# Optimization experiments

Hardware: AMD Instinct MI355X
Metric: run time of the kernel (lower is better)

The kernel has to match this reference:

```python
import jax, jax.numpy as jnp
import numpy as np

B, O, D = 4096, 256, 256  # batch, size_out (rules), size_in (features)


def setup_inputs() -> dict:
    key = jax.random.key(0)
    k1, k2, k3, k4, k5 = jax.random.split(key, 5)
    return {
        "x": jax.random.normal(k1, (B, D), dtype=jnp.float32),
        "scales": jax.random.normal(k2, (O, D), dtype=jnp.float32),
        # strict upper triangle holds the packed rot vectors (original inits them to zeros;
        # small values keep the quadratic form well conditioned)
        "rots": jax.random.normal(k3, (O, D, D), dtype=jnp.float32) * 0.02,
        "centroids": jax.random.normal(k4, (O, D, 1), dtype=jnp.float32),
        "b": jax.random.uniform(k5, (O,), dtype=jnp.float32, minval=0.5, maxval=1.5),
    }


def reference(x, scales, rots, centroids, b):
    # Build symmetric transform A[o] = diag(scales[o]) + triu(rots[o],1) + triu(rots[o],1)^T
    # (equivalent to the loop of diag_embed(r_i, i+1) + mirrored lower diagonal).
    upper = jnp.triu(rots, 1)                                   # [O,D,D]
    A = upper + jnp.swapaxes(upper, -1, -2)
    A = A + jnp.eye(D, dtype=scales.dtype) * scales[:, None, :]  # diag_embed(scales)
    # Augmented affine map: mul[o,i,b'] = A[o] @ x[b'] + centroid[o,i]; const row dropped
    # since only the first size_in rows feed the norm.
    y = jnp.einsum('bj,oij->boi', x, A) + centroids[..., 0][None, :, :]  # [B,O,D]
    rx = jnp.sqrt(jnp.sum(y * y, axis=-1))                      # L2 norm over D -> [B,O]
    return 1.0 / (1.0 + rx ** (2.0 * b))                        # bell membership [B,O]
```

## Files before the change

### kernel.cpp

```cpp
#include <hip/hip_runtime.h>
#include <cstdint>
#include <cmath>

#define Bn 4096
#define Dn 256
#define On 256

typedef __bf16 v8bf __attribute__((ext_vector_type(8)));
typedef float  v16f __attribute__((ext_vector_type(16)));
typedef unsigned short us8 __attribute__((ext_vector_type(8)));

__device__ __forceinline__ unsigned short f2bf(float f) {
    unsigned int u = __builtin_bit_cast(unsigned int, f);
    unsigned int r = (u + 0x7fffu + ((u >> 16) & 1u)) >> 16;
    return (unsigned short)r;
}

__device__ __forceinline__ void gl_lds16(const void* g, void* l) {
    __builtin_amdgcn_global_load_lds(
        (const __attribute__((address_space(1))) void*)(uintptr_t)g,
        (__attribute__((address_space(3))) void*)(uintptr_t)l, 16, 0, 0);
}

__global__ __launch_bounds__(256) void prep_x(const float* __restrict__ x,
                                              unsigned short* __restrict__ xbT) {
    __shared__ float t[64][68];
    const int tid = threadIdx.x;
    const int bb = blockIdx.x >> 2;
    const int kb = blockIdx.x & 3;
    const int b0 = bb * 64;
#pragma unroll
    for (int s = 0; s < 4; ++s) {
        const int idx = s * 256 + tid;
        const int r = idx >> 4, c4 = idx & 15;
        const float4 v = *(const float4*)(x + (size_t)(b0 + r) * Dn + kb * 64 + c4 * 4);
        *(float4*)&t[r][c4 * 4] = v;
    }
    __syncthreads();
    const int lane = tid & 63, wv = tid >> 6;
#pragma unroll
    for (int s = 0; s < 2; ++s) {
        const int kcl = s * 4 + wv;
        us8 u;
#pragma unroll
        for (int q = 0; q < 8; ++q) u[q] = f2bf(t[lane][kcl * 8 + q]);
        *(us8*)(xbT + ((size_t)(kb * 8 + kcl) * Bn + b0 + lane) * 8) = u;
    }
}

template <int TI, int TJ>
__device__ __forceinline__ void extract_pair(const float* T, v8bf (&af)[2][16],
                                             const float (&sc2)[2],
                                             int wv, int lane) {
    const int l31 = lane & 31, hw = lane >> 5;
    if (TI == TJ) {
        if (wv == TI) {
#pragma unroll
            for (int mt = 0; mt < 2; ++mt) {
                const int r = mt * 32 + l31;
                const int mr = (r & 7) << 2;
#pragma unroll
                for (int kq = 0; kq < 4; ++kq) {
                    us8 u;
#pragma unroll
                    for (int q = 0; q < 8; ++q) {
                        const int c = kq * 16 + hw * 8 + q;
                        const float v = (r < c) ? T[r * 64 + (c ^ mr)]
                                      : ((r > c) ? T[c * 64 + (r ^ ((c & 7) << 2))]
                                                 : sc2[mt]);
                        u[q] = f2bf(v);
                    }
                    af[mt][TJ * 4 + kq] = __builtin_bit_cast(v8bf, u);
                }
            }
        }
    } else {
        if (wv == TI) {
#pragma unroll
            for (int mt = 0; mt < 2; ++mt) {
                const int r = mt * 32 + l31;
                const int mr = (r & 7) << 2;
#pragma unroll
                for (int kq = 0; kq < 4; ++kq) {
                    const int c0 = kq * 16 + hw * 8;
                    const float4 a = *(const float4*)&T[r * 64 + (c0 ^ mr)];
                    const float4 b = *(const float4*)&T[r * 64 + ((c0 + 4) ^ mr)];
                    us8 u;
                    u[0] = f2bf(a.x); u[1] = f2bf(a.y); u[2] = f2bf(a.z); u[3] = f2bf(a.w);
                    u[4] = f2bf(b.x); u[5] = f2bf(b.y); u[6] = f2bf(b.z); u[7] = f2bf(b.w);
                    af[mt][TJ * 4 + kq] = __builtin_bit_cast(v8bf, u);
                }
            }
        } else if (wv == TJ) {
#pragma unroll
            for (int mt = 0; mt < 2; ++mt) {
                const int cL = mt * 32 + l31;
#pragma unroll
                for (int kq = 0; kq < 4; ++kq) {
                    us8 u;
#pragma unroll
                    for (int q = 0; q < 8; ++q) {
                        const int rL = kq * 16 + hw * 8 + q;
                        u[q] = f2bf(T[rL * 64 + (cL ^ ((rL & 7) << 2))]);
                    }
                    af[mt][TI * 4 + kq] = __builtin_bit_cast(v8bf, u);
                }
            }
        }
    }
}

#define WAITV(N)                                              \
    do {                                                      \
        asm volatile("s_waitcnt vmcnt(" #N ")" ::: "memory"); \
        __builtin_amdgcn_sched_barrier(0);                    \
    } while (0)
#define LGKM0()                                               \
    do {                                                      \
        asm volatile("s_waitcnt lgkmcnt(0)" ::: "memory");    \
        __builtin_amdgcn_sched_barrier(0);                    \
    } while (0)
#define BARF()                                                \
    do {                                                      \
        __builtin_amdgcn_sched_barrier(0);                    \
        __builtin_amdgcn_s_barrier();                         \
        __builtin_amdgcn_sched_barrier(0);                    \
    } while (0)

#define STAGE_T(TIv, TJv, DST)                                               \
    do {                                                                     \
        const float* s_ = rbase + (TIv) * (64 * Dn) + (TJv) * 64;            \
        _Pragma("unroll")                                                    \
        for (int s = 0; s < 4; ++s) {                                        \
            const int idx = s * 256 + tid;                                   \
            const int r = idx >> 4, c4 = idx & 15;                           \
            gl_lds16(s_ + (size_t)r * Dn + ((c4 ^ (r & 7)) * 4),             \
                     (DST) + idx * 4);                                       \
        }                                                                    \
    } while (0)

#define XSTAGE(BUF, B0)                                                      \
    do {                                                                     \
        _Pragma("unroll")                                                    \
        for (int s = 0; s < 8; ++s) {                                        \
            gl_lds16(xbT + ((size_t)(s * 4 + wv) * Bn + (B0) + lane) * 8,    \
                     &Xs[BUF][s * 256 + tid][0]);                            \
        }                                                                    \
    } while (0)

__global__ __launch_bounds__(256, 2) void fuzzy_main(
    const float* __restrict__ rots, const float* __restrict__ scales,
    const unsigned short* __restrict__ xbT, const float* __restrict__ cent,
    const float* __restrict__ bvals, float* __restrict__ out) {
    __shared__ __align__(16) unsigned short Xs[2][2048][8];
    __shared__ float ssbuf[2][4][64];
    __shared__ float centL[Dn];

    const int tid  = threadIdx.x;
    const int lane = tid & 63;
    const int wv   = tid >> 6;
    const int l31  = lane & 31, hw = lane >> 5;
    const int Lb = blockIdx.x;
    const int o     = (Lb & 7) * 32 + ((Lb >> 3) & 31);
    const int bhalf = Lb >> 8;

    centL[tid] = cent[o * Dn + tid];
    float sc2[2];
#pragma unroll
    for (int mt = 0; mt < 2; ++mt)
        sc2[mt] = scales[o * Dn + wv * 64 + mt * 32 + l31];
    const float bv = bvals[o];

    WAITV(0);

    float* const S0 = (float*)&Xs[1][0][0];
    float* const S1 = S0 + 4096;
    float* const S2 = (float*)&Xs[0][0][0];
    float* const S3 = S2 + 4096;
    const float* const rbase = rots + ((size_t)o << 16);

    v8bf af[2][16];

    STAGE_T(0, 1, S0); STAGE_T(2, 3, S1);
    STAGE_T(0, 2, S2); STAGE_T(1, 3, S3);
    WAITV(8); BARF();
    extract_pair<0, 1>(S0, af, sc2, wv, lane);
    extract_pair<2, 3>(S1, af, sc2, wv, lane);
    LGKM0(); BARF();
    STAGE_T(0, 3, S0); STAGE_T(1, 2, S1);
    WAITV(8); BARF();
    extract_pair<0, 2>(S2, af, sc2, wv, lane);
    extract_pair<1, 3>(S3, af, sc2, wv, lane);
    LGKM0(); BARF();
    STAGE_T(0, 0, S2); STAGE_T(1, 1, S3);
    WAITV(8); BARF();
    extract_pair<0, 3>(S0, af, sc2, wv, lane);
    extract_pair<1, 2>(S1, af, sc2, wv, lane);
    LGKM0(); BARF();
    STAGE_T(2, 2, S0); STAGE_T(3, 3, S1);
    WAITV(8); BARF();
    extract_pair<0, 0>(S2, af, sc2, wv, lane);
    extract_pair<1, 1>(S3, af, sc2, wv, lane);
    LGKM0(); BARF();
    WAITV(0); BARF();
    extract_pair<2, 2>(S0, af, sc2, wv, lane);
    extract_pair<3, 3>(S1, af, sc2, wv, lane);
    LGKM0(); BARF();

    XSTAGE(0, bhalf * 2048);
    __syncthreads();

    for (int it = 0; it < 32; ++it) {
        const int buf = it & 1;
        const int b0  = bhalf * 2048 + it * 64;
        if (it < 31) XSTAGE(buf ^ 1, b0 + 64);

        if (it > 0 && lane < 16) {
            const int bl = wv * 16 + lane;
            const float ssq = ssbuf[buf ^ 1][0][bl] + ssbuf[buf ^ 1][1][bl] +
                              ssbuf[buf ^ 1][2][bl] + ssbuf[buf ^ 1][3][bl];
            out[(size_t)(b0 - 64 + bl) * On + o] =
                1.0f / (1.0f + exp2f(bv * log2f(ssq)));
        }

        v16f acc[2][2];
#pragma unroll
        for (int mt = 0; mt < 2; ++mt)
#pragma unroll
            for (int nt = 0; nt < 2; ++nt)
#pragma unroll
                for (int rg = 0; rg < 16; ++rg) acc[mt][nt][rg] = 0.f;

#pragma unroll
        for (int ks = 0; ks < 16; ++ks) {
            v8bf xf[2];
#pragma unroll
            for (int nt = 0; nt < 2; ++nt)
                xf[nt] = *(const v8bf*)&Xs[buf][(ks * 2 + hw) * 64 + nt * 32 + l31][0];
#pragma unroll
            for (int mt = 0; mt < 2; ++mt)
#pragma unroll
                for (int nt = 0; nt < 2; ++nt)
                    acc[mt][nt] = __builtin_amdgcn_mfma_f32_32x32x16_bf16(
                        af[mt][ks], xf[nt], acc[mt][nt], 0, 0, 0);
        }

#pragma unroll
        for (int nt = 0; nt < 2; ++nt) {
            float v = 0.f;
#pragma unroll
            for (int mt = 0; mt < 2; ++mt)
#pragma unroll
                for (int rg = 0; rg < 16; ++rg) {
                    const float y = acc[mt][nt][rg] +
                        centL[wv * 64 + mt * 32 + (rg & 3) + 8 * (rg >> 2) + 4 * hw];
                    v += y * y;
                }
            v += __shfl_xor(v, 32);
            if (lane < 32) ssbuf[buf][wv][nt * 32 + lane] = v;
        }
        __syncthreads();
    }
    if (lane < 16) {
        const int bl = wv * 16 + lane;
        const float ssq = ssbuf[1][0][bl] + ssbuf[1][1][bl] +
                          ssbuf[1][2][bl] + ssbuf[1][3][bl];
        out[(size_t)(bhalf * 2048 + 31 * 64 + bl) * On + o] =
            1.0f / (1.0f + exp2f(bv * log2f(ssq)));
    }
}

__global__ void fallback_kernel(const float* __restrict__ x, const float* __restrict__ scales,
                                const float* __restrict__ rots, const float* __restrict__ cent,
                                const float* __restrict__ bvals, float* __restrict__ out) {
    const int b = blockIdx.x * blockDim.x + threadIdx.x;
    const int o = blockIdx.y;
    if (b >= Bn) return;
    const float* R  = rots + (size_t)o * Dn * Dn;
    const float* xv = x + (size_t)b * Dn;
    float ss = 0.f;
    for (int i = 0; i < Dn; ++i) {
        float a = cent[o * Dn + i];
        for (int j = 0; j < Dn; ++j) {
            const float w = (j > i) ? R[i * Dn + j]
                          : ((j < i) ? R[j * Dn + i] : scales[o * Dn + i]);
            a += w * xv[j];
        }
        ss += a * a;
    }
    out[(size_t)b * On + o] = 1.f / (1.f + powf(ss, bvals[o]));
}

extern "C" void kernel_launch(void* const* d_in, const int* in_sizes, int n_in,
                              void* d_out, int out_size, void* d_ws, size_t ws_size,
                              hipStream_t stream) {
    const float* x         = (const float*)d_in[0];
    const float* scales    = (const float*)d_in[1];
    const float* rots      = (const float*)d_in[2];
    const float* centroids = (const float*)d_in[3];
    const float* bvals     = (const float*)d_in[4];
    float* out = (float*)d_out;

    const size_t needX = (size_t)Bn * Dn * sizeof(unsigned short);

    if (ws_size >= needX) {
        unsigned short* xbT = (unsigned short*)d_ws;
        prep_x<<<dim3(256), 256, 0, stream>>>(x, xbT);
        fuzzy_main<<<dim3(512), 256, 0, stream>>>(rots, scales, xbT, centroids, bvals, out);
    } else {
        fallback_kernel<<<dim3(Bn / 256, On), 256, 0, stream>>>(x, scales, rots, centroids,
                                                                bvals, out);
    }
}
```

Before: 225.9 us.

## Software-pipeline MFMA tiles with epilogue norm reduction across iterations

The main loop now splits each 64-column batch tile into two 32-column halves. The squared-norm epilogue of one half's accumulators is interleaved with the MFMA chain of the other half, so VALU work overlaps matrix-core work instead of running after it. The partial-sum buffer becomes triple-buffered to carry results across iterations. The X staging pointers are precomputed and incremented to cut address arithmetic. This adds a skewed prologue and epilogue and keeps an extra accumulator live across iterations, which raises register pressure.

Measured after the change: 224.5 us. Within noise of the previous version (-0.6%).

```diff
diff --git a/kernel.cpp b/kernel.cpp
--- a/kernel.cpp
+++ b/kernel.cpp
@@ -139,21 +139,12 @@
         }                                                                    \
     } while (0)
 
-#define XSTAGE(BUF, B0)                                                      \
-    do {                                                                     \
-        _Pragma("unroll")                                                    \
-        for (int s = 0; s < 8; ++s) {                                        \
-            gl_lds16(xbT + ((size_t)(s * 4 + wv) * Bn + (B0) + lane) * 8,    \
-                     &Xs[BUF][s * 256 + tid][0]);                            \
-        }                                                                    \
-    } while (0)
-
 __global__ __launch_bounds__(256, 2) void fuzzy_main(
     const float* __restrict__ rots, const float* __restrict__ scales,
     const unsigned short* __restrict__ xbT, const float* __restrict__ cent,
     const float* __restrict__ bvals, float* __restrict__ out) {
     __shared__ __align__(16) unsigned short Xs[2][2048][8];
-    __shared__ float ssbuf[2][4][64];
+    __shared__ float ssbuf[3][4][64];
     __shared__ float centL[Dn];
 
     const int tid  = threadIdx.x;
@@ -163,6 +154,7 @@
     const int Lb = blockIdx.x;
     const int o     = (Lb & 7) * 32 + ((Lb >> 3) & 31);
     const int bhalf = Lb >> 8;
+    const int bh0   = bhalf * 2048;
 
     centL[tid] = cent[o * Dn + tid];
     float sc2[2];
@@ -207,66 +199,129 @@
     extract_pair<3, 3>(S1, af, sc2, wv, lane);
     LGKM0(); BARF();
 
-    XSTAGE(0, bhalf * 2048);
+    const unsigned short* px[8];
+#pragma unroll
+    for (int s = 0; s < 8; ++s)
+        px[s] = xbT + ((size_t)(s * 4 + wv) * Bn + bh0 + lane) * 8;
+
+#pragma unroll
+    for (int s = 0; s < 8; ++s)
+        gl_lds16(px[s], &Xs[0][s * 256 + tid][0]);
     __syncthreads();
 
+    v16f acc1[2];
+#pragma unroll
+    for (int mt = 0; mt < 2; ++mt)
+#pragma unroll
+        for (int rg = 0; rg < 16; ++rg) acc1[mt][rg] = 0.f;
+
     for (int it = 0; it < 32; ++it) {
-        const int buf = it & 1;
-        const int b0  = bhalf * 2048 + it * 64;
-        if (it < 31) XSTAGE(buf ^ 1, b0 + 64);
-
-        if (it > 0 && lane < 16) {
+        const int buf  = it & 1;
+        const int parc = it % 3;
+        const int parp = (it + 2) % 3;
+
+        if (it < 31) {
+#pragma unroll
+            for (int s = 0; s < 8; ++s) {
+                px[s] += 512;
+                gl_lds16(px[s], &Xs[buf ^ 1][s * 256 + tid][0]);
+            }
+        }
+
+        if (it >= 2 && lane < 16) {
+            const int paro = (it + 1) % 3;
             const int bl = wv * 16 + lane;
-            const float ssq = ssbuf[buf ^ 1][0][bl] + ssbuf[buf ^ 1][1][bl] +
-                              ssbuf[buf ^ 1][2][bl] + ssbuf[buf ^ 1][3][bl];
-            out[(size_t)(b0 - 64 + bl) * On + o] =
+            const float ssq = ssbuf[paro][0][bl] + ssbuf[paro][1][bl] +
+                              ssbuf[paro][2][bl] + ssbuf[paro][3][bl];
+            out[(size_t)(bh0 + (it - 2) * 64 + bl) * On + o] =
                 1.0f / (1.0f + exp2f(bv * log2f(ssq)));
         }
 
-        v16f acc[2][2];
+        v16f acc0[2];
 #pragma unroll
         for (int mt = 0; mt < 2; ++mt)
 #pragma unroll
-            for (int nt = 0; nt < 2; ++nt)
-#pragma unroll
-                for (int rg = 0; rg < 16; ++rg) acc[mt][nt][rg] = 0.f;
-
+            for (int rg = 0; rg < 16; ++rg) acc0[mt][rg] = 0.f;
+
+        float p0 = 0.f, p1 = 0.f;
+        float4 c4p;
 #pragma unroll
         for (int ks = 0; ks < 16; ++ks) {
-            v8bf xf[2];
-#pragma unroll
-            for (int nt = 0; nt < 2; ++nt)
-                xf[nt] = *(const v8bf*)&Xs[buf][(ks * 2 + hw) * 64 + nt * 32 + l31][0];
-#pragma unroll
-            for (int mt = 0; mt < 2; ++mt)
-#pragma unroll
-                for (int nt = 0; nt < 2; ++nt)
-                    acc[mt][nt] = __builtin_amdgcn_mfma_f32_32x32x16_bf16(
-                        af[mt][ks], xf[nt], acc[mt][nt], 0, 0, 0);
-        }
-
-#pragma unroll
-        for (int nt = 0; nt < 2; ++nt) {
-            float v = 0.f;
-#pragma unroll
-            for (int mt = 0; mt < 2; ++mt)
-#pragma unroll
-                for (int rg = 0; rg < 16; ++rg) {
-                    const float y = acc[mt][nt][rg] +
-                        centL[wv * 64 + mt * 32 + (rg & 3) + 8 * (rg >> 2) + 4 * hw];
-                    v += y * y;
+            const v8bf xf0 = *(const v8bf*)&Xs[buf][(ks * 2 + hw) * 64 + l31][0];
+            acc0[0] = __builtin_amdgcn_mfma_f32_32x32x16_bf16(af[0][ks], xf0, acc0[0], 0, 0, 0);
+            acc0[1] = __builtin_amdgcn_mfma_f32_32x32x16_bf16(af[1][ks], xf0, acc0[1], 0, 0, 0);
+            const int mt = ks >> 3, rg0 = (2 * ks) & 15;
+            if ((ks & 1) == 0)
+                c4p = *(const float4*)&centL[wv * 64 + mt * 32 + 8 * (rg0 >> 2) + 4 * hw];
+            const float y0 = acc1[mt][rg0]     + ((ks & 1) ? c4p.z : c4p.x);
+            const float y1 = acc1[mt][rg0 + 1] + ((ks & 1) ? c4p.w : c4p.y);
+            p0 = fmaf(y0, y0, p0);
+            p1 = fmaf(y1, y1, p1);
+        }
+        {
+            float v1 = p0 + p1;
+            v1 += __shfl_xor(v1, 32);
+            if (lane < 32) ssbuf[parp][wv][32 + lane] = v1;
+        }
+
+#pragma unroll
+        for (int mt = 0; mt < 2; ++mt)
+#pragma unroll
+            for (int rg = 0; rg < 16; ++rg) acc1[mt][rg] = 0.f;
+
+        float q0 = 0.f, q1 = 0.f;
+        float4 c4c;
+#pragma unroll
+        for (int ks = 0; ks < 16; ++ks) {
+            const v8bf xf1 = *(const v8bf*)&Xs[buf][(ks * 2 + hw) * 64 + 32 + l31][0];
+            acc1[0] = __builtin_amdgcn_mfma_f32_32x32x16_bf16(af[0][ks], xf1, acc1[0], 0, 0, 0);
+            acc1[1] = __builtin_amdgcn_mfma_f32_32x32x16_bf16(af[1][ks], xf1, acc1[1], 0, 0, 0);
+            const int mt = ks >> 3, rg0 = (2 * ks) & 15;
+            if ((ks & 1) == 0)
+                c4c = *(const float4*)&centL[wv * 64 + mt * 32 + 8 * (rg0 >> 2) + 4 * hw];
+            const float y0 = acc0[mt][rg0]     + ((ks & 1) ? c4c.z : c4c.x);
+            const float y1 = acc0[mt][rg0 + 1] + ((ks & 1) ? c4c.w : c4c.y);
+            q0 = fmaf(y0, y0, q0);
+            q1 = fmaf(y1, y1, q1);
+        }
+        {
+            float v0 = q0 + q1;
+            v0 += __shfl_xor(v0, 32);
+            if (lane < 32) ssbuf[parc][wv][lane] = v0;
+        }
+
+        __syncthreads();
+    }
+
+    {
+        float p0 = 0.f, p1 = 0.f;
+#pragma unroll
+        for (int mt = 0; mt < 2; ++mt)
+#pragma unroll
+            for (int g = 0; g < 4; ++g) {
+                const float4 c4 = *(const float4*)&centL[wv * 64 + mt * 32 + 8 * g + 4 * hw];
+#pragma unroll
+                for (int pq = 0; pq < 4; ++pq) {
+                    const float y = acc1[mt][g * 4 + pq] +
+                        ((pq == 0) ? c4.x : (pq == 1) ? c4.y : (pq == 2) ? c4.z : c4.w);
+                    if (pq & 1) p1 = fmaf(y, y, p1); else p0 = fmaf(y, y, p0);
                 }
-            v += __shfl_xor(v, 32);
-            if (lane < 32) ssbuf[buf][wv][nt * 32 + lane] = v;
-        }
-        __syncthreads();
-    }
+            }
+        float v1 = p0 + p1;
+        v1 += __shfl_xor(v1, 32);
+        if (lane < 32) ssbuf[31 % 3][wv][32 + lane] = v1;
+    }
+    __syncthreads();
     if (lane < 16) {
         const int bl = wv * 16 + lane;
-        const float ssq = ssbuf[1][0][bl] + ssbuf[1][1][bl] +
-                          ssbuf[1][2][bl] + ssbuf[1][3][bl];
-        out[(size_t)(bhalf * 2048 + 31 * 64 + bl) * On + o] =
-            1.0f / (1.0f + exp2f(bv * log2f(ssq)));
+#pragma unroll
+        for (int j = 30; j <= 31; ++j) {
+            const int par = j % 3;
+            const float ssq = ssbuf[par][0][bl] + ssbuf[par][1][bl] +
+                              ssbuf[par][2][bl] + ssbuf[par][3][bl];
+            out[(size_t)(bh0 + j * 64 + bl) * On + o] =
+                1.0f / (1.0f + exp2f(bv * log2f(ssq)));
+        }
     }
 }
 
```

## Split each rule's A rows across eight waves with 512-thread blocks

Applied to the files above, without the earlier changes.

Doubles the block to 512 threads so each wave holds 32 rows of the per-rule A matrix (16 bf16 fragments) instead of 64, which halves the register footprint per wave and raises occupancy through launch_bounds(512,4). The tile staging, the x prefetch into LDS, and the row-sum reduction are rebalanced for eight waves. The centroid add now uses float4 LDS reads and fma. In exchange, each wave reuses each LDS-loaded x fragment for fewer MFMAs, so LDS traffic per MFMA doubles, and the final reduction sums eight partials instead of four.

Result: slower. 236.2 us (+4.6%).

```diff
diff --git a/kernel.cpp b/kernel.cpp
--- a/kernel.cpp
+++ b/kernel.cpp
@@ -49,62 +49,53 @@
 }
 
 template <int TI, int TJ>
-__device__ __forceinline__ void extract_pair(const float* T, v8bf (&af)[2][16],
-                                             const float (&sc2)[2],
-                                             int wv, int lane) {
+__device__ __forceinline__ void extract_pair(const float* T, v8bf (&af)[16],
+                                             float sc, int wv, int lane) {
     const int l31 = lane & 31, hw = lane >> 5;
+    const int half = wv & 1, grp = wv >> 1;
     if (TI == TJ) {
-        if (wv == TI) {
-#pragma unroll
-            for (int mt = 0; mt < 2; ++mt) {
-                const int r = mt * 32 + l31;
-                const int mr = (r & 7) << 2;
-#pragma unroll
-                for (int kq = 0; kq < 4; ++kq) {
-                    us8 u;
-#pragma unroll
-                    for (int q = 0; q < 8; ++q) {
-                        const int c = kq * 16 + hw * 8 + q;
-                        const float v = (r < c) ? T[r * 64 + (c ^ mr)]
-                                      : ((r > c) ? T[c * 64 + (r ^ ((c & 7) << 2))]
-                                                 : sc2[mt]);
-                        u[q] = f2bf(v);
-                    }
-                    af[mt][TJ * 4 + kq] = __builtin_bit_cast(v8bf, u);
+        if (grp == TI) {
+            const int r = half * 32 + l31;
+            const int mr = (r & 7) << 2;
+#pragma unroll
+            for (int kq = 0; kq < 4; ++kq) {
+                us8 u;
+#pragma unroll
+                for (int q = 0; q < 8; ++q) {
+                    const int c = kq * 16 + hw * 8 + q;
+                    const float v = (r < c) ? T[r * 64 + (c ^ mr)]
+                                  : ((r > c) ? T[c * 64 + (r ^ ((c & 7) << 2))]
+                                             : sc);
+                    u[q] = f2bf(v);
                 }
+                af[TI * 4 + kq] = __builtin_bit_cast(v8bf, u);
             }
         }
     } else {
-        if (wv == TI) {
-#pragma unroll
-            for (int mt = 0; mt < 2; ++mt) {
-                const int r = mt * 32 + l31;
-                const int mr = (r & 7) << 2;
-#pragma unroll
-                for (int kq = 0; kq < 4; ++kq) {
-                    const int c0 = kq * 16 + hw * 8;
-                    const float4 a = *(const float4*)&T[r * 64 + (c0 ^ mr)];
-                    const float4 b = *(const float4*)&T[r * 64 + ((c0 + 4) ^ mr)];
-                    us8 u;
-                    u[0] = f2bf(a.x); u[1] = f2bf(a.y); u[2] = f2bf(a.z); u[3] = f2bf(a.w);
-                    u[4] = f2bf(b.x); u[5] = f2bf(b.y); u[6] = f2bf(b.z); u[7] = f2bf(b.w);
-                    af[mt][TJ * 4 + kq] = __builtin_bit_cast(v8bf, u);
+        if (grp == TI) {
+            const int r = half * 32 + l31;
+            const int mr = (r & 7) << 2;
+#pragma unroll
+            for (int kq = 0; kq < 4; ++kq) {
+                const int c0 = kq * 16 + hw * 8;
+                const float4 a = *(const float4*)&T[r * 64 + (c0 ^ mr)];
+                const float4 b = *(const float4*)&T[r * 64 + ((c0 + 4) ^ mr)];
+                us8 u;
+                u[0] = f2bf(a.x); u[1] = f2bf(a.y); u[2] = f2bf(a.z); u[3] = f2bf(a.w);
+                u[4] = f2bf(b.x); u[5] = f2bf(b.y); u[6] = f2bf(b.z); u[7] = f2bf(b.w);
+                af[TJ * 4 + kq] = __builtin_bit_cast(v8bf, u);
+            }
+        } else if (grp == TJ) {
+            const int cL = half * 32 + l31;
+#pragma unroll
+            for (int kq = 0; kq < 4; ++kq) {
+                us8 u;
+#pragma unroll
+                for (int q = 0; q < 8; ++q) {
+                    const int rL = kq * 16 + hw * 8 + q;
+                    u[q] = f2bf(T[rL * 64 + (cL ^ ((rL & 7) << 2))]);
                 }
-            }
-        } else if (wv == TJ) {
-#pragma unroll
-            for (int mt = 0; mt < 2; ++mt) {
-                const int cL = mt * 32 + l31;
-#pragma unroll
-                for (int kq = 0; kq < 4; ++kq) {
-                    us8 u;
-#pragma unroll
-                    for (int q = 0; q < 8; ++q) {
-                        const int rL = kq * 16 + hw * 8 + q;
-                        u[q] = f2bf(T[rL * 64 + (cL ^ ((rL & 7) << 2))]);
-                    }
-                    af[mt][TI * 4 + kq] = __builtin_bit_cast(v8bf, u);
-                }
+                af[TI * 4 + kq] = __builtin_bit_cast(v8bf, u);
             }
         }
     }
@@ -131,29 +122,20 @@
     do {                                                                     \
         const float* s_ = rbase + (TIv) * (64 * Dn) + (TJv) * 64;            \
         _Pragma("unroll")                                                    \
-        for (int s = 0; s < 4; ++s) {                                        \
-            const int idx = s * 256 + tid;                                   \
+        for (int s = 0; s < 2; ++s) {                                        \
+            const int idx = s * 512 + tid;                                   \
             const int r = idx >> 4, c4 = idx & 15;                           \
             gl_lds16(s_ + (size_t)r * Dn + ((c4 ^ (r & 7)) * 4),             \
                      (DST) + idx * 4);                                       \
         }                                                                    \
     } while (0)
 
-#define XSTAGE(BUF, B0)                                                      \
-    do {                                                                     \
-        _Pragma("unroll")                                                    \
-        for (int s = 0; s < 8; ++s) {                                        \
-            gl_lds16(xbT + ((size_t)(s * 4 + wv) * Bn + (B0) + lane) * 8,    \
-                     &Xs[BUF][s * 256 + tid][0]);                            \
-        }                                                                    \
-    } while (0)
-
-__global__ __launch_bounds__(256, 2) void fuzzy_main(
+__global__ __launch_bounds__(512, 4) void fuzzy_main(
     const float* __restrict__ rots, const float* __restrict__ scales,
     const unsigned short* __restrict__ xbT, const float* __restrict__ cent,
     const float* __restrict__ bvals, float* __restrict__ out) {
     __shared__ __align__(16) unsigned short Xs[2][2048][8];
-    __shared__ float ssbuf[2][4][64];
+    __shared__ float ssbuf[2][8][64];
     __shared__ float centL[Dn];
 
     const int tid  = threadIdx.x;
@@ -163,109 +145,114 @@
     const int Lb = blockIdx.x;
     const int o     = (Lb & 7) * 32 + ((Lb >> 3) & 31);
     const int bhalf = Lb >> 8;
-
-    centL[tid] = cent[o * Dn + tid];
-    float sc2[2];
-#pragma unroll
-    for (int mt = 0; mt < 2; ++mt)
-        sc2[mt] = scales[o * Dn + wv * 64 + mt * 32 + l31];
+    const int bh0   = bhalf * 2048;
+
+    if (tid < Dn) centL[tid] = cent[o * Dn + tid];
+    const float sc = scales[o * Dn + wv * 32 + l31];
     const float bv = bvals[o];
 
     WAITV(0);
 
-    float* const S0 = (float*)&Xs[1][0][0];
+    float* const S0 = (float*)&Xs[0][0][0];
     float* const S1 = S0 + 4096;
-    float* const S2 = (float*)&Xs[0][0][0];
+    float* const S2 = (float*)&Xs[1][0][0];
     float* const S3 = S2 + 4096;
     const float* const rbase = rots + ((size_t)o << 16);
 
-    v8bf af[2][16];
+    v8bf af[16];
 
     STAGE_T(0, 1, S0); STAGE_T(2, 3, S1);
     STAGE_T(0, 2, S2); STAGE_T(1, 3, S3);
-    WAITV(8); BARF();
-    extract_pair<0, 1>(S0, af, sc2, wv, lane);
-    extract_pair<2, 3>(S1, af, sc2, wv, lane);
+    WAITV(4); BARF();
+    extract_pair<0, 1>(S0, af, sc, wv, lane);
+    extract_pair<2, 3>(S1, af, sc, wv, lane);
     LGKM0(); BARF();
     STAGE_T(0, 3, S0); STAGE_T(1, 2, S1);
-    WAITV(8); BARF();
-    extract_pair<0, 2>(S2, af, sc2, wv, lane);
-    extract_pair<1, 3>(S3, af, sc2, wv, lane);
+    WAITV(4); BARF();
+    extract_pair<0, 2>(S2, af, sc, wv, lane);
+    extract_pair<1, 3>(S3, af, sc, wv, lane);
     LGKM0(); BARF();
     STAGE_T(0, 0, S2); STAGE_T(1, 1, S3);
-    WAITV(8); BARF();
-    extract_pair<0, 3>(S0, af, sc2, wv, lane);
-    extract_pair<1, 2>(S1, af, sc2, wv, lane);
+    WAITV(4); BARF();
+    extract_pair<0, 3>(S0, af, sc, wv, lane);
+    extract_pair<1, 2>(S1, af, sc, wv, lane);
     LGKM0(); BARF();
     STAGE_T(2, 2, S0); STAGE_T(3, 3, S1);
-    WAITV(8); BARF();
-    extract_pair<0, 0>(S2, af, sc2, wv, lane);
-    extract_pair<1, 1>(S3, af, sc2, wv, lane);
+    WAITV(4); BARF();
+    extract_pair<0, 0>(S2, af, sc, wv, lane);
+    extract_pair<1, 1>(S3, af, sc, wv, lane);
     LGKM0(); BARF();
     WAITV(0); BARF();
-    extract_pair<2, 2>(S0, af, sc2, wv, lane);
-    extract_pair<3, 3>(S1, af, sc2, wv, lane);
-    LGKM0(); BARF();
-
-    XSTAGE(0, bhalf * 2048);
+    extract_pair<2, 2>(S0, af, sc, wv, lane);
+    extract_pair<3, 3>(S1, af, sc, wv, lane);
+    LGKM0(); BARF();
+
+    const unsigned short* px[4];
+#pragma unroll
+    for (int s = 0; s < 4; ++s)
+        px[s] = xbT + ((size_t)(s * 8 + wv) * Bn + bh0 + lane) * 8;
+
+#pragma unroll
+    for (int s = 0; s < 4; ++s)
+        gl_lds16(px[s], &Xs[0][s * 512 + tid][0]);
     __syncthreads();
 
     for (int it = 0; it < 32; ++it) {
         const int buf = it & 1;
-        const int b0  = bhalf * 2048 + it * 64;
-        if (it < 31) XSTAGE(buf ^ 1, b0 + 64);
-
-        if (it > 0 && lane < 16) {
-            const int bl = wv * 16 + lane;
-            const float ssq = ssbuf[buf ^ 1][0][bl] + ssbuf[buf ^ 1][1][bl] +
-                              ssbuf[buf ^ 1][2][bl] + ssbuf[buf ^ 1][3][bl];
-            out[(size_t)(b0 - 64 + bl) * On + o] =
+        if (it < 31) {
+#pragma unroll
+            for (int s = 0; s < 4; ++s) {
+                px[s] += 512;
+                gl_lds16(px[s], &Xs[buf ^ 1][s * 512 + tid][0]);
+            }
+        }
+
+        if (it >= 1 && lane < 8) {
+            const int bl = wv * 8 + lane;
+            float ssq = 0.f;
+#pragma unroll
+            for (int w = 0; w < 8; ++w) ssq += ssbuf[buf ^ 1][w][bl];
+            out[(size_t)(bh0 + (it - 1) * 64 + bl) * On + o] =
                 1.0f / (1.0f + exp2f(bv * log2f(ssq)));
         }
 
-        v16f acc[2][2];
-#pragma unroll
-        for (int mt = 0; mt < 2; ++mt)
-#pragma unroll
-            for (int nt = 0; nt < 2; ++nt)
-#pragma unroll
-                for (int rg = 0; rg < 16; ++rg) acc[mt][nt][rg] = 0.f;
+        v16f acc[2];
+#pragma unroll
+        for (int nt = 0; nt < 2; ++nt)
+#pragma unroll
+            for (int rg = 0; rg < 16; ++rg) acc[nt][rg] = 0.f;
 
 #pragma unroll
         for (int ks = 0; ks < 16; ++ks) {
-            v8bf xf[2];
-#pragma unroll
-            for (int nt = 0; nt < 2; ++nt)
-                xf[nt] = *(const v8bf*)&Xs[buf][(ks * 2 + hw) * 64 + nt * 32 + l31][0];
-#pragma unroll
-            for (int mt = 0; mt < 2; ++mt)
-#pragma unroll
-                for (int nt = 0; nt < 2; ++nt)
-                    acc[mt][nt] = __builtin_amdgcn_mfma_f32_32x32x16_bf16(
-                        af[mt][ks], xf[nt], acc[mt][nt], 0, 0, 0);
+            const v8bf xf0 = *(const v8bf*)&Xs[buf][(ks * 2 + hw) * 64 + l31][0];
+            const v8bf xf1 = *(const v8bf*)&Xs[buf][(ks * 2 + hw) * 64 + 32 + l31][0];
+            acc[0] = __builtin_amdgcn_mfma_f32_32x32x16_bf16(af[ks], xf0, acc[0], 0, 0, 0);
+            acc[1] = __builtin_amdgcn_mfma_f32_32x32x16_bf16(af[ks], xf1, acc[1], 0, 0, 0);
         }
 
 #pragma unroll
         for (int nt = 0; nt < 2; ++nt) {
             float v = 0.f;
 #pragma unroll
-            for (int mt = 0; mt < 2; ++mt)
-#pragma unroll
-                for (int rg = 0; rg < 16; ++rg) {
-                    const float y = acc[mt][nt][rg] +
-                        centL[wv * 64 + mt * 32 + (rg & 3) + 8 * (rg >> 2) + 4 * hw];
-                    v += y * y;
-                }
+            for (int g = 0; g < 4; ++g) {
+                const float4 c4 = *(const float4*)&centL[wv * 32 + 8 * g + 4 * hw];
+                float y;
+                y = acc[nt][g * 4 + 0] + c4.x; v = fmaf(y, y, v);
+                y = acc[nt][g * 4 + 1] + c4.y; v = fmaf(y, y, v);
+                y = acc[nt][g * 4 + 2] + c4.z; v = fmaf(y, y, v);
+                y = acc[nt][g * 4 + 3] + c4.w; v = fmaf(y, y, v);
+            }
             v += __shfl_xor(v, 32);
             if (lane < 32) ssbuf[buf][wv][nt * 32 + lane] = v;
         }
         __syncthreads();
     }
-    if (lane < 16) {
-        const int bl = wv * 16 + lane;
-        const float ssq = ssbuf[1][0][bl] + ssbuf[1][1][bl] +
-                          ssbuf[1][2][bl] + ssbuf[1][3][bl];
-        out[(size_t)(bhalf * 2048 + 31 * 64 + bl) * On + o] =
+    if (lane < 8) {
+        const int bl = wv * 8 + lane;
+        float ssq = 0.f;
+#pragma unroll
+        for (int w = 0; w < 8; ++w) ssq += ssbuf[1][w][bl];
+        out[(size_t)(bh0 + 31 * 64 + bl) * On + o] =
             1.0f / (1.0f + exp2f(bv * log2f(ssq)));
     }
 }
@@ -306,7 +293,7 @@
     if (ws_size >= needX) {
         unsigned short* xbT = (unsigned short*)d_ws;
         prep_x<<<dim3(256), 256, 0, stream>>>(x, xbT);
-        fuzzy_main<<<dim3(512), 256, 0, stream>>>(rots, scales, xbT, centroids, bvals, out);
+        fuzzy_main<<<dim3(512), 512, 0, stream>>>(rots, scales, xbT, centroids, bvals, out);
     } else {
         fallback_kernel<<<dim3(Bn / 256, On), 256, 0, stream>>>(x, scales, rots, centroids,
                                                                 bvals, out);
```

## Restructure x staging into 4-slot ring of 32-column tiles with pointer increments

Applied to the files above, without the earlier changes.

Splits each 64-column batch tile into two 32-column sub-tiles held in a 4-slot LDS ring. Global addresses are kept as per-thread pointers that are simply advanced each step, and prefetch runs two sub-tiles ahead. Each wave now uses 2 MFMA accumulators per sub-tile instead of 4, and the centroid add is vectorized with float4 LDS reads. The MFMA loop is wrapped in s_setprio, and output writes are batched every other iteration with an extra barrier. The aim is to cut accumulator register pressure and address arithmetic and to overlap loads better. In exchange it issues more frequent full waits and barriers.

New measurement: 219.6 us. 1.03x faster.

```diff
diff --git a/kernel.cpp b/kernel.cpp
--- a/kernel.cpp
+++ b/kernel.cpp
@@ -139,12 +139,12 @@
         }                                                                    \
     } while (0)
 
-#define XSTAGE(BUF, B0)                                                      \
+#define STAGE_X(BUF)                                                         \
     do {                                                                     \
         _Pragma("unroll")                                                    \
-        for (int s = 0; s < 8; ++s) {                                        \
-            gl_lds16(xbT + ((size_t)(s * 4 + wv) * Bn + (B0) + lane) * 8,    \
-                     &Xs[BUF][s * 256 + tid][0]);                            \
+        for (int s = 0; s < 4; ++s) {                                        \
+            gl_lds16(px[s], &Xs[BUF][s * 256 + tid][0]);                     \
+            px[s] += 256;                  \
         }                                                                    \
     } while (0)
 
@@ -152,8 +152,8 @@
     const float* __restrict__ rots, const float* __restrict__ scales,
     const unsigned short* __restrict__ xbT, const float* __restrict__ cent,
     const float* __restrict__ bvals, float* __restrict__ out) {
-    __shared__ __align__(16) unsigned short Xs[2][2048][8];
-    __shared__ float ssbuf[2][4][64];
+    __shared__ __align__(16) unsigned short Xs[4][1024][8];
+    __shared__ float ssbuf[4][4][32];
     __shared__ float centL[Dn];
 
     const int tid  = threadIdx.x;
@@ -163,6 +163,7 @@
     const int Lb = blockIdx.x;
     const int o     = (Lb & 7) * 32 + ((Lb >> 3) & 31);
     const int bhalf = Lb >> 8;
+    const int bh0   = bhalf * 2048;
 
     centL[tid] = cent[o * Dn + tid];
     float sc2[2];
@@ -173,10 +174,10 @@
 
     WAITV(0);
 
-    float* const S0 = (float*)&Xs[1][0][0];
-    float* const S1 = S0 + 4096;
-    float* const S2 = (float*)&Xs[0][0][0];
-    float* const S3 = S2 + 4096;
+    float* const S0 = (float*)&Xs[0][0][0];
+    float* const S1 = (float*)&Xs[1][0][0];
+    float* const S2 = (float*)&Xs[2][0][0];
+    float* const S3 = (float*)&Xs[3][0][0];
     const float* const rbase = rots + ((size_t)o << 16);
 
     v8bf af[2][16];
@@ -207,66 +208,68 @@
     extract_pair<3, 3>(S1, af, sc2, wv, lane);
     LGKM0(); BARF();
 
-    XSTAGE(0, bhalf * 2048);
-    __syncthreads();
-
-    for (int it = 0; it < 32; ++it) {
-        const int buf = it & 1;
-        const int b0  = bhalf * 2048 + it * 64;
-        if (it < 31) XSTAGE(buf ^ 1, b0 + 64);
-
-        if (it > 0 && lane < 16) {
-            const int bl = wv * 16 + lane;
-            const float ssq = ssbuf[buf ^ 1][0][bl] + ssbuf[buf ^ 1][1][bl] +
-                              ssbuf[buf ^ 1][2][bl] + ssbuf[buf ^ 1][3][bl];
-            out[(size_t)(b0 - 64 + bl) * On + o] =
-                1.0f / (1.0f + exp2f(bv * log2f(ssq)));
-        }
-
-        v16f acc[2][2];
-#pragma unroll
-        for (int mt = 0; mt < 2; ++mt)
-#pragma unroll
-            for (int nt = 0; nt < 2; ++nt)
-#pragma unroll
-                for (int rg = 0; rg < 16; ++rg) acc[mt][nt][rg] = 0.f;
-
-#pragma unroll
-        for (int ks = 0; ks < 16; ++ks) {
-            v8bf xf[2];
-#pragma unroll
-            for (int nt = 0; nt < 2; ++nt)
-                xf[nt] = *(const v8bf*)&Xs[buf][(ks * 2 + hw) * 64 + nt * 32 + l31][0];
-#pragma unroll
-            for (int mt = 0; mt < 2; ++mt)
-#pragma unroll
-                for (int nt = 0; nt < 2; ++nt)
-                    acc[mt][nt] = __builtin_amdgcn_mfma_f32_32x32x16_bf16(
-                        af[mt][ks], xf[nt], acc[mt][nt], 0, 0, 0);
-        }
-
-#pragma unroll
-        for (int nt = 0; nt < 2; ++nt) {
+    const unsigned short* px[4];
+#pragma unroll
+    for (int s = 0; s < 4; ++s) {
+        const int idx = s * 256 + tid;
+        px[s] = xbT + ((size_t)(idx >> 5) * Bn + bh0 + (idx & 31)) * 8;
+    }
+
+    STAGE_X(0); STAGE_X(1);
+    WAITV(0); LGKM0(); BARF();
+
+    for (int p = 0; p < 32; ++p) {
+        const int t0 = 2 * p;
+        if (p < 31) { STAGE_X((t0 + 2) & 3); STAGE_X((t0 + 3) & 3); }
+
+#pragma unroll
+        for (int s = 0; s < 2; ++s) {
+            const int t = t0 + s;
+            const int buf = t & 3;
+
+            v16f a0, a1;
+#pragma unroll
+            for (int rg = 0; rg < 16; ++rg) { a0[rg] = 0.f; a1[rg] = 0.f; }
+            __builtin_amdgcn_s_setprio(1);
+#pragma unroll
+            for (int ks = 0; ks < 16; ++ks) {
+                const v8bf xf = *(const v8bf*)&Xs[buf][(ks * 2 + hw) * 32 + l31][0];
+                a0 = __builtin_amdgcn_mfma_f32_32x32x16_bf16(af[0][ks], xf, a0, 0, 0, 0);
+                a1 = __builtin_amdgcn_mfma_f32_32x32x16_bf16(af[1][ks], xf, a1, 0, 0, 0);
+            }
+            __builtin_amdgcn_s_setprio(0);
+
             float v = 0.f;
 #pragma unroll
-            for (int mt = 0; mt < 2; ++mt)
-#pragma unroll
-                for (int rg = 0; rg < 16; ++rg) {
-                    const float y = acc[mt][nt][rg] +
-                        centL[wv * 64 + mt * 32 + (rg & 3) + 8 * (rg >> 2) + 4 * hw];
-                    v += y * y;
-                }
+            for (int g = 0; g < 4; ++g) {
+                const float4 c0 = *(const float4*)&centL[wv * 64 + 8 * g + 4 * hw];
+                const float4 c1 = *(const float4*)&centL[wv * 64 + 32 + 8 * g + 4 * hw];
+                float y;
+                y = a0[g * 4 + 0] + c0.x; v = fmaf(y, y, v);
+                y = a0[g * 4 + 1] + c0.y; v = fmaf(y, y, v);
+                y = a0[g * 4 + 2] + c0.z; v = fmaf(y, y, v);
+                y = a0[g * 4 + 3] + c0.w; v = fmaf(y, y, v);
+                y = a1[g * 4 + 0] + c1.x; v = fmaf(y, y, v);
+                y = a1[g * 4 + 1] + c1.y; v = fmaf(y, y, v);
+                y = a1[g * 4 + 2] + c1.z; v = fmaf(y, y, v);
+                y = a1[g * 4 + 3] + c1.w; v = fmaf(y, y, v);
+            }
             v += __shfl_xor(v, 32);
-            if (lane < 32) ssbuf[buf][wv][nt * 32 + lane] = v;
-        }
-        __syncthreads();
-    }
-    if (lane < 16) {
-        const int bl = wv * 16 + lane;
-        const float ssq = ssbuf[1][0][bl] + ssbuf[1][1][bl] +
-                          ssbuf[1][2][bl] + ssbuf[1][3][bl];
-        out[(size_t)(bhalf * 2048 + 31 * 64 + bl) * On + o] =
-            1.0f / (1.0f + exp2f(bv * log2f(ssq)));
+            if (lane < 32) ssbuf[t & 3][wv][l31] = v;
+        }
+
+        WAITV(0); LGKM0(); BARF();
+
+        if ((p & 1) == 1) {
+            const int tb = (p >> 1) * 4 + wv;
+            if (lane < 32) {
+                float ssq = ssbuf[wv][0][l31] + ssbuf[wv][1][l31] +
+                            ssbuf[wv][2][l31] + ssbuf[wv][3][l31];
+                out[(size_t)(bh0 + tb * 32 + l31) * On + o] =
+                    1.0f / (1.0f + exp2f(bv * log2f(ssq)));
+            }
+            LGKM0(); BARF();
+        }
     }
 }
 
```
